# Kernel tuning notes

Hardware: AMD Instinct MI355X
Metric: run time of the kernel (lower is better)

## Reference

```python
import jax, jax.numpy as jnp
import numpy as np

B, C, H, W, K = 4, 64, 128, 128, 3
K2 = K * K
PAD = (K - 1) // 2  # same padding for 3x3


def setup_inputs() -> dict:
    key = jax.random.key(0)
    ks = jax.random.split(key, 9)
    s = 0.05
    return {
        "x": jax.random.normal(ks[0], (B, C, H, W), jnp.float32),
        "inter": jax.random.normal(ks[1], (B, C, H, W), jnp.float32),
        # offset/mask predictor conv: input cat([x, inter]) -> 3*K2 channels (dy, dx, mask)
        "w_offset": jax.random.normal(ks[2], (3 * K2, 2 * C, K, K), jnp.float32) * s,
        "b_offset": jnp.zeros((3 * K2,), jnp.float32),
        # deformable conv weight (bias=False per DGM init)
        "w_dcn": jax.random.normal(ks[3], (C, C, K, K), jnp.float32) * s,
        # SFT gamma branch: two 1x1 convs (bias=False)
        "w_g1": jax.random.normal(ks[4], (C, C), jnp.float32) * s,
        "w_g2": jax.random.normal(ks[5], (C, C), jnp.float32) * s,
        # SFT beta branch: two 1x1 convs (bias=False)
        "w_b1": jax.random.normal(ks[6], (C, C), jnp.float32) * s,
        "w_b2": jax.random.normal(ks[7], (C, C), jnp.float32) * s,
    }


def _lrelu(v):
    # LeakyReLU(0.1)
    return jnp.where(v >= 0, v, 0.1 * v)


def _conv(x, w, b=None):
    y = jax.lax.conv_general_dilated(
        x, w, window_strides=(1, 1), padding=[(PAD, PAD), (PAD, PAD)],
        dimension_numbers=("NCHW", "OIHW", "NCHW"))
    if b is not None:
        y = y + b[None, :, None, None]
    return y


def _bilinear_gather(x, py, px):
    """x: [B,C,H,W]; py, px: [B,K2,H,W] float sample coords.
    Returns samples [B,K2,H,W,C]; out-of-bounds treated as zero (DCN zero-pad)."""
    y0 = jnp.floor(py)
    x0 = jnp.floor(px)
    wy = (py - y0)[..., None]
    wx = (px - x0)[..., None]

    def gather(yi, xi):
        valid = ((yi >= 0) & (yi < H) & (xi >= 0) & (xi < W)).astype(x.dtype)
        yc = jnp.clip(yi, 0, H - 1).astype(jnp.int32)
        xc = jnp.clip(xi, 0, W - 1).astype(jnp.int32)
        bidx = jnp.arange(B)[:, None, None, None]
        v = x[bidx, :, yc, xc]  # advanced indexing -> [B,K2,H,W,C]
        return v * valid[..., None]

    v00 = gather(y0, x0)
    v01 = gather(y0, x0 + 1)
    v10 = gather(y0 + 1, x0)
    v11 = gather(y0 + 1, x0 + 1)
    return (v00 * (1 - wy) * (1 - wx) + v01 * (1 - wy) * wx
            + v10 * wy * (1 - wx) + v11 * wy * wx)


def _dgm_forward(x, inter, w_offset, b_offset, w_dcn, w_g1, w_g2, w_b1, w_b2):
    # --- WADCN branch: modulated deformable conv, offsets predicted from cat(x, inter)
    om = _conv(jnp.concatenate([x, inter], axis=1), w_offset, b_offset)  # [B,3K2,H,W]
    dy, dx, m = jnp.split(om, 3, axis=1)  # each [B,K2,H,W]
    mask = jax.nn.sigmoid(m)

    ky, kx = jnp.meshgrid(jnp.arange(K), jnp.arange(K), indexing="ij")
    ky = ky.reshape(K2).astype(x.dtype)
    kx = kx.reshape(K2).astype(x.dtype)
    hh = jnp.arange(H, dtype=x.dtype)
    ww = jnp.arange(W, dtype=x.dtype)
    # sample coords: base grid + kernel-tap offset + learned offset
    py = hh[None, None, :, None] + (ky - PAD)[None, :, None, None] + dy  # [B,K2,H,W]
    px = ww[None, None, None, :] + (kx - PAD)[None, :, None, None] + dx

    samp = _bilinear_gather(x, py, px) * mask[..., None]  # [B,K2,H,W,C]
    dcn_out = jnp.einsum("bkhwc,ock->bohw", samp, w_dcn.reshape(C, C, K2))

    # --- SFT branch: two 1x1-conv + LeakyReLU chains producing gamma/beta
    gamma = jnp.einsum("oc,bchw->bohw", w_g2,
                       _lrelu(jnp.einsum("oc,bchw->bohw", w_g1, inter)))
    beta = jnp.einsum("oc,bchw->bohw", w_b2,
                      _lrelu(jnp.einsum("oc,bchw->bohw", w_b1, inter)))
    sft_out = x * gamma + beta

    # --- fused residual combine (DGM.relu is defined but never applied)
    return x + dcn_out + sft_out


def reference(x, inter, w_offset, b_offset, w_dcn, w_g1, w_g2, w_b1, w_b2):
    return _dgm_forward(x, inter, w_offset, b_offset, w_dcn, w_g1, w_g2, w_b1, w_b2)
```

## Files before the change

kernel.cpp:

```cpp
#include <hip/hip_runtime.h>
#include <hip/hip_bf16.h>
#include <math.h>

#define BB 4
#define CC 64
#define HH 128
#define WW 128
#define HW (HH*WW)
#define NPIX (BB*HW)

typedef __attribute__((ext_vector_type(8))) short short8;
typedef __attribute__((ext_vector_type(4))) float f32x4;

__device__ __forceinline__ float bf2f(ushort u) {
  union { unsigned u; float f; } v; v.u = ((unsigned)u) << 16; return v.f;
}
__device__ __forceinline__ ushort f2bf(float f) {
  __hip_bfloat16 h = __float2bfloat16(f); return *(ushort*)&h;
}

__global__ __launch_bounds__(256) void k_prep(
    const float* __restrict__ x, const float* __restrict__ inter,
    const float* __restrict__ w_off, const float* __restrict__ w_dcn,
    const float* __restrict__ wg1, const float* __restrict__ wb1,
    const float* __restrict__ wg2, const float* __restrict__ wb2,
    ushort* __restrict__ x_clh, ushort* __restrict__ inter_clh,
    ushort* __restrict__ wfb, ushort* __restrict__ wdT,
    ushort* __restrict__ w1gb, ushort* __restrict__ w1bb,
    ushort* __restrict__ w2gb, ushort* __restrict__ w2bb,
    float* __restrict__ zp) {
  __shared__ __align__(16) float tile[64 * 128];
  int blk = blockIdx.x;
  int tid = threadIdx.x;
  if (blk < 1024) {
    int sel = blk >> 9;
    int bh = blk & 511;
    int b = bh >> 7, h = bh & 127;
    const float* src = sel ? inter : x;
    ushort* dst = sel ? inter_clh : x_clh;
    const float* sp = src + (size_t)(b * 64) * HW + h * WW;
#pragma unroll
    for (int it = 0; it < 8; ++it) {
      int idx = it * 256 + tid;
      int c = idx >> 5, wq = idx & 31;
      float4 v = *(const float4*)(sp + (size_t)c * HW + wq * 4);
      int s = (c >> 3) & 7;
      *(float4*)(&tile[c * 128 + ((wq ^ s) << 2)]) = v;
    }
    __syncthreads();
    ushort* dp = dst + ((size_t)b * HW + h * WW) * 64;
#pragma unroll
    for (int it = 0; it < 4; ++it) {
      int idx = it * 256 + tid;
      int w = idx >> 3, c8 = idx & 7;
      short8 outv;
#pragma unroll
      for (int j = 0; j < 8; ++j) {
        int c = c8 * 8 + j;
        int sl = (w >> 2) ^ c8;
        float f = tile[c * 128 + (sl << 2) + (w & 3)];
        outv[j] = (short)f2bf(f);
      }
      *(short8*)(dp + (size_t)w * 64 + c8 * 8) = outv;
    }
  } else if (blk < 1168) {
    int i = (blk - 1024) * 256 + tid;
    if (i < 64) zp[i] = 0.f;
    if (i < 9 * 32 * 128) {
      int tap = i >> 12, rem = i & 4095, m = rem >> 7, c = rem & 127;
      float v = (m < 27) ? w_off[(size_t)(m * 128 + c) * 9 + tap] : 0.f;
      wfb[i] = f2bf(v);
    }
  } else if (blk < 1312) {
    int i = (blk - 1168) * 256 + tid;
    if (i < 64 * 64 * 9) {
      int o = i / 576, rem = i % 576, k = rem >> 6, c = rem & 63;
      wdT[i] = f2bf(w_dcn[(o * 64 + c) * 9 + k]);
    }
  } else {
    int i = (blk - 1312) * 256 + tid;
    int m = i >> 12, j = i & 4095;
    const float* src = (m == 0) ? wg1 : (m == 1) ? wb1 : (m == 2) ? wg2 : wb2;
    ushort* dst = (m == 0) ? w1gb : (m == 1) ? w1bb : (m == 2) ? w2gb : w2bb;
    dst[j] = f2bf(src[j]);
  }
}

#define SPITCH 196
#define NPX 32
#define FPX 72

__global__ __launch_bounds__(256, 6) void k_omega(
    const float* __restrict__ x, const ushort* __restrict__ x_clh,
    const ushort* __restrict__ inter_clh,
    const float* __restrict__ b_off, const ushort* __restrict__ wfb,
    const ushort* __restrict__ wdT,
    const ushort* __restrict__ w1gb, const ushort* __restrict__ w1bb,
    const ushort* __restrict__ w2gb, const ushort* __restrict__ w2bb,
    const ushort* __restrict__ zp16, float* __restrict__ out) {
  __shared__ __align__(16) ushort LDSB[9792];
  ushort* S  = LDSB;
  ushort* Sg = LDSB;
  ushort* Sb = LDSB + NPX * FPX;
  int*   cycx = (int*)(LDSB + 6272);
  float* cwy  = (float*)(LDSB + 6848);
  float* cwx  = (float*)(LDSB + 7424);
  float* oml  = (float*)(LDSB + 8000);

  int tid = threadIdx.x;
  int wave = tid >> 6, lane = tid & 63;
  int quad = lane >> 4, col = lane & 15;
  int rr = lane >> 3, g = lane & 7;
  int bid = blockIdx.x;
  int wid = (bid & 7) * 256 + (bid >> 3);
  int pg0 = wid * NPX;
  int b = pg0 >> 14, hw0 = pg0 & 16383;
  int h = hw0 >> 7, w0 = hw0 & 127;
  int pt = wave >> 1, mt = wave & 1;
  int o_base = __builtin_amdgcn_readfirstlane(wave * 16);

  f32x4 accx = {0.f, 0.f, 0.f, 0.f}, acci = {0.f, 0.f, 0.f, 0.f};
  {
    const ushort* wb0 = wfb + (size_t)(mt * 16 + col) * 128 + quad * 8;
    int pxcol = pt * 16 + col;
    unsigned bbase = (unsigned)b * HW;
#pragma unroll 1
    for (int ky = 0; ky < 3; ++ky) {
      int hs = h + ky - 1;
      bool oky = (unsigned)hs < 128u;
      int rowb = hs << 7;
#pragma unroll
      for (int kx = 0; kx < 3; ++kx) {
        int ws = w0 + pxcol + kx - 1;
        bool ok = oky && ((unsigned)ws < 128u);
        long long poff = (long long)(int)(bbase + rowb + ws) * 64;
        const ushort* bx = (ok ? x_clh + poff : zp16) + quad * 8;
        const ushort* bi = (ok ? inter_clh + poff : zp16) + quad * 8;
        const ushort* wt = wb0 + (size_t)(ky * 3 + kx) * 4096;
#pragma unroll
        for (int ks = 0; ks < 2; ++ks) {
          short8 a0 = *(const short8*)(wt + ks * 32);
          short8 b0 = *(const short8*)(bx + ks * 32);
          accx = __builtin_amdgcn_mfma_f32_16x16x32_bf16(a0, b0, accx, 0, 0, 0);
          short8 a1 = *(const short8*)(wt + 64 + ks * 32);
          short8 b1 = *(const short8*)(bi + ks * 32);
          acci = __builtin_amdgcn_mfma_f32_16x16x32_bf16(a1, b1, acci, 0, 0, 0);
        }
      }
    }
  }
#pragma unroll
  for (int r = 0; r < 4; ++r) {
    int o = mt * 16 + quad * 4 + r;
    if (o < 27) oml[o * 33 + pt * 16 + col] = accx[r] + acci[r];
  }

  f32x4 ag[2], ab[2];
#pragma unroll
  for (int nt = 0; nt < 2; ++nt) {
    ag[nt] = (f32x4){0.f, 0.f, 0.f, 0.f};
    ab[nt] = (f32x4){0.f, 0.f, 0.f, 0.f};
  }
#pragma unroll
  for (int ks = 0; ks < 2; ++ks) {
    short8 a_g = *(const short8*)(w1gb + (size_t)(o_base + col) * 64 + ks * 32 + quad * 8);
    short8 a_b = *(const short8*)(w1bb + (size_t)(o_base + col) * 64 + ks * 32 + quad * 8);
#pragma unroll
    for (int nt = 0; nt < 2; ++nt) {
      short8 bf = *(const short8*)(inter_clh + (size_t)(pg0 + nt * 16 + col) * 64 + ks * 32 + quad * 8);
      ag[nt] = __builtin_amdgcn_mfma_f32_16x16x32_bf16(a_g, bf, ag[nt], 0, 0, 0);
      ab[nt] = __builtin_amdgcn_mfma_f32_16x16x32_bf16(a_b, bf, ab[nt], 0, 0, 0);
    }
  }
#pragma unroll
  for (int nt = 0; nt < 2; ++nt) {
    int px = nt * 16 + col;
    ushort pkg[4], pkb[4];
#pragma unroll
    for (int r = 0; r < 4; ++r) {
      float vg = ag[nt][r]; vg = vg >= 0.f ? vg : 0.1f * vg;
      float vb = ab[nt][r]; vb = vb >= 0.f ? vb : 0.1f * vb;
      pkg[r] = f2bf(vg); pkb[r] = f2bf(vb);
    }
    *(uint2*)(&Sg[px * FPX + o_base + quad * 4]) = *(uint2*)pkg;
    *(uint2*)(&Sb[px * FPX + o_base + quad * 4]) = *(uint2*)pkb;
  }
  __syncthreads();

  f32x4 gg[2], gb[2];
#pragma unroll
  for (int nt = 0; nt < 2; ++nt) {
    gg[nt] = (f32x4){0.f, 0.f, 0.f, 0.f};
    gb[nt] = (f32x4){0.f, 0.f, 0.f, 0.f};
  }
#pragma unroll
  for (int ks = 0; ks < 2; ++ks) {
    short8 a_g = *(const short8*)(w2gb + (size_t)(o_base + col) * 64 + ks * 32 + quad * 8);
    short8 a_b = *(const short8*)(w2bb + (size_t)(o_base + col) * 64 + ks * 32 + quad * 8);
#pragma unroll
    for (int nt = 0; nt < 2; ++nt) {
      short8 bgf = *(const short8*)(Sg + (nt * 16 + col) * FPX + ks * 32 + quad * 8);
      short8 bbf = *(const short8*)(Sb + (nt * 16 + col) * FPX + ks * 32 + quad * 8);
      gg[nt] = __builtin_amdgcn_mfma_f32_16x16x32_bf16(a_g, bgf, gg[nt], 0, 0, 0);
      gb[nt] = __builtin_amdgcn_mfma_f32_16x16x32_bf16(a_b, bbf, gb[nt], 0, 0, 0);
    }
  }
  float ev[2][4];
#pragma unroll
  for (int nt = 0; nt < 2; ++nt)
#pragma unroll
    for (int r = 0; r < 4; ++r) {
      int o = o_base + quad * 4 + r;
      float xv = x[(size_t)(b * 64 + o) * HW + hw0 + nt * 16 + col];
      ev[nt][r] = xv + xv * gg[nt][r] + gb[nt][r];
    }

  for (int i = tid; i < 9 * NPX; i += 256) {
    int k = i >> 5, p = i & 31;
    float dy = oml[k * 33 + p] + b_off[k];
    float dx = oml[(9 + k) * 33 + p] + b_off[9 + k];
    float mz = oml[(18 + k) * 33 + p] + b_off[18 + k];
    float py = (float)(h + (k / 3) - 1) + dy;
    float px = (float)(w0 + p + (k % 3) - 1) + dx;
    float y0f = floorf(py), x0f = floorf(px);
    int iy = (int)y0f, ix = (int)x0f;
    cycx[i] = (iy & 0xffff) | (ix << 16);
    cwy[i] = py - y0f;
    cwx[i] = px - x0f;
    oml[(18 + k) * 33 + p] = 1.f / (1.f + __expf(-mz));
  }

  f32x4 acc[2];
  acc[0] = (f32x4){0.f, 0.f, 0.f, 0.f};
  acc[1] = (f32x4){0.f, 0.f, 0.f, 0.f};

  const ushort* bp = x_clh + (size_t)b * HW * 64;
  int p = wave * 8 + rr;

#pragma unroll 1
  for (int chunk = 0; chunk < 3; ++chunk) {
    __syncthreads();
#pragma unroll
    for (int it = 0; it < 3; ++it) {
      int k = chunk * 3 + it;
      int idx = k * 32 + p;
      int v = cycx[idx];
      int y0 = (int)(short)(v & 0xffff);
      int x0 = v >> 16;
      float wy = cwy[idx], wx = cwx[idx];
      float m = oml[(18 + k) * 33 + p];
      bool yok0 = (unsigned)y0 < 128u, yok1 = (unsigned)(y0 + 1) < 128u;
      bool xok0 = (unsigned)x0 < 128u, xok1 = (unsigned)(x0 + 1) < 128u;
      const ushort* r0 = bp + ((size_t)(int)((y0 << 7) + x0)) * 64 + g * 8;
      const ushort* r1 = r0 + (size_t)WW * 64;
      short8 s00 = *(const short8*)((yok0 && xok0) ? r0 : zp16);
      short8 s01 = *(const short8*)((yok0 && xok1) ? (r0 + 64) : zp16);
      short8 s10 = *(const short8*)((yok1 && xok0) ? r1 : zp16);
      short8 s11 = *(const short8*)((yok1 && xok1) ? (r1 + 64) : zp16);
      short8 outv;
#pragma unroll
      for (int j = 0; j < 8; ++j) {
        float v00 = bf2f((ushort)s00[j]), v01 = bf2f((ushort)s01[j]);
        float v10 = bf2f((ushort)s10[j]), v11 = bf2f((ushort)s11[j]);
        float top = v00 + (v01 - v00) * wx;
        float bot = v10 + (v11 - v10) * wx;
        float val = top + (bot - top) * wy;
        outv[j] = (short)f2bf(val * m);
      }
      *(short8*)(&S[p * SPITCH + it * 64 + g * 8]) = outv;
    }
    __syncthreads();
    const ushort* wrow = wdT + (size_t)(o_base + col) * 576 + chunk * 192 + quad * 8;
    const ushort* srow = S + quad * 8;
#pragma unroll
    for (int ks = 0; ks < 6; ++ks) {
      short8 a = *(const short8*)(wrow + ks * 32);
#pragma unroll
      for (int nt = 0; nt < 2; ++nt) {
        short8 bf = *(const short8*)(srow + (nt * 16 + col) * SPITCH + ks * 32);
        acc[nt] = __builtin_amdgcn_mfma_f32_16x16x32_bf16(a, bf, acc[nt], 0, 0, 0);
      }
    }
  }

#pragma unroll
  for (int nt = 0; nt < 2; ++nt) {
#pragma unroll
    for (int r = 0; r < 4; ++r) {
      int o = o_base + quad * 4 + r;
      size_t idx = (size_t)(b * 64 + o) * HW + hw0 + nt * 16 + col;
      out[idx] = ev[nt][r] + acc[nt][r];
    }
  }
}

extern "C" void kernel_launch(void* const* d_in, const int* in_sizes, int n_in,
                              void* d_out, int out_size, void* d_ws, size_t ws_size,
                              hipStream_t stream) {
  const float* x     = (const float*)d_in[0];
  const float* inter = (const float*)d_in[1];
  const float* w_off = (const float*)d_in[2];
  const float* b_off = (const float*)d_in[3];
  const float* w_dcn = (const float*)d_in[4];
  const float* wg1   = (const float*)d_in[5];
  const float* wg2   = (const float*)d_in[6];
  const float* wb1   = (const float*)d_in[7];
  const float* wb2   = (const float*)d_in[8];
  float* out = (float*)d_out;

  float* ws        = (float*)d_ws;
  ushort* x_clh    = (ushort*)ws;
  ushort* inter_clh= (ushort*)(ws + 2097152);
  ushort* wfb      = (ushort*)(ws + 4194304);
  ushort* wdT      = (ushort*)(ws + 4212736);
  ushort* w1gb     = (ushort*)(ws + 4231168);
  ushort* w1bb     = (ushort*)(ws + 4233216);
  ushort* w2gb     = (ushort*)(ws + 4235264);
  ushort* w2bb     = (ushort*)(ws + 4237312);
  float* zp        = ws + 4239360;

  k_prep<<<1376, 256, 0, stream>>>(x, inter, w_off, w_dcn, wg1, wb1, wg2, wb2,
                                   x_clh, inter_clh, wfb, wdT,
                                   w1gb, w1bb, w2gb, w2bb, zp);

  k_omega<<<2048, 256, 0, stream>>>(x, x_clh, inter_clh, b_off, wfb, wdT,
                                    w1gb, w1bb, w2gb, w2bb,
                                    (const ushort*)zp, out);
}
```

Measured before the change: 204.1 us.

## Give each wave its own pixel tile and feed bilinear samples straight into MFMA

Each block now covers 64 pixels instead of 32, and each wave owns 16 pixels across all 64 output channels, where before the waves split the work by output channel. The bilinear samples are built in registers in the MFMA B-operand layout and consumed directly, which removes the LDS staging buffer and the per-chunk barriers in the deformable-conv loop. The offset conv and SFT stages are reorganised the same way, with fewer blocks and launch bounds reduced to 4 blocks per SIMD. The cost is more accumulator registers per wave and possibly lower occupancy, and every wave now reloads all the weight rows from global memory or cache.

```diff
diff --git a/kernel.cpp b/kernel.cpp
--- a/kernel.cpp
+++ b/kernel.cpp
@@ -86,11 +86,11 @@
   }
 }
 
-#define SPITCH 196
-#define NPX 32
-#define FPX 72
-
-__global__ __launch_bounds__(256, 6) void k_omega(
+#define NPX 64
+#define SGP 72
+#define OMP 66
+
+__global__ __launch_bounds__(256, 4) void k_omega(
     const float* __restrict__ x, const ushort* __restrict__ x_clh,
     const ushort* __restrict__ inter_clh,
     const float* __restrict__ b_off, const ushort* __restrict__ wfb,
@@ -98,200 +98,191 @@
     const ushort* __restrict__ w1gb, const ushort* __restrict__ w1bb,
     const ushort* __restrict__ w2gb, const ushort* __restrict__ w2bb,
     const ushort* __restrict__ zp16, float* __restrict__ out) {
-  __shared__ __align__(16) ushort LDSB[9792];
-  ushort* S  = LDSB;
+  __shared__ __align__(16) ushort LDSB[12780];
   ushort* Sg = LDSB;
-  ushort* Sb = LDSB + NPX * FPX;
-  int*   cycx = (int*)(LDSB + 6272);
-  float* cwy  = (float*)(LDSB + 6848);
-  float* cwx  = (float*)(LDSB + 7424);
-  float* oml  = (float*)(LDSB + 8000);
+  ushort* Sb = LDSB + 4608;
+  int*   cycx = (int*)LDSB;
+  float* cwy  = (float*)(LDSB + 1152);
+  float* cwx  = (float*)(LDSB + 2304);
+  float* oml  = (float*)(LDSB + 9216);
 
   int tid = threadIdx.x;
   int wave = tid >> 6, lane = tid & 63;
   int quad = lane >> 4, col = lane & 15;
-  int rr = lane >> 3, g = lane & 7;
   int bid = blockIdx.x;
-  int wid = (bid & 7) * 256 + (bid >> 3);
+  int wid = (bid & 7) * 128 + (bid >> 3);
   int pg0 = wid * NPX;
   int b = pg0 >> 14, hw0 = pg0 & 16383;
   int h = hw0 >> 7, w0 = hw0 & 127;
-  int pt = wave >> 1, mt = wave & 1;
-  int o_base = __builtin_amdgcn_readfirstlane(wave * 16);
-
-  f32x4 accx = {0.f, 0.f, 0.f, 0.f}, acci = {0.f, 0.f, 0.f, 0.f};
+  int pxl = wave * 16 + col;
+  int pxg = pg0 + pxl;
+
+  f32x4 am0 = {0.f, 0.f, 0.f, 0.f}, am1 = {0.f, 0.f, 0.f, 0.f};
   {
-    const ushort* wb0 = wfb + (size_t)(mt * 16 + col) * 128 + quad * 8;
-    int pxcol = pt * 16 + col;
+    const ushort* wb0 = wfb + (size_t)col * 128 + quad * 8;
+    const ushort* wb1 = wfb + (size_t)(16 + col) * 128 + quad * 8;
     unsigned bbase = (unsigned)b * HW;
-#pragma unroll 1
+#pragma unroll
     for (int ky = 0; ky < 3; ++ky) {
       int hs = h + ky - 1;
       bool oky = (unsigned)hs < 128u;
       int rowb = hs << 7;
 #pragma unroll
       for (int kx = 0; kx < 3; ++kx) {
-        int ws = w0 + pxcol + kx - 1;
+        int ws = w0 + pxl + kx - 1;
         bool ok = oky && ((unsigned)ws < 128u);
         long long poff = (long long)(int)(bbase + rowb + ws) * 64;
         const ushort* bx = (ok ? x_clh + poff : zp16) + quad * 8;
         const ushort* bi = (ok ? inter_clh + poff : zp16) + quad * 8;
-        const ushort* wt = wb0 + (size_t)(ky * 3 + kx) * 4096;
+        int tap = ky * 3 + kx;
+        const ushort* wt0 = wb0 + (size_t)tap * 4096;
+        const ushort* wt1 = wb1 + (size_t)tap * 4096;
 #pragma unroll
         for (int ks = 0; ks < 2; ++ks) {
-          short8 a0 = *(const short8*)(wt + ks * 32);
           short8 b0 = *(const short8*)(bx + ks * 32);
-          accx = __builtin_amdgcn_mfma_f32_16x16x32_bf16(a0, b0, accx, 0, 0, 0);
-          short8 a1 = *(const short8*)(wt + 64 + ks * 32);
           short8 b1 = *(const short8*)(bi + ks * 32);
-          acci = __builtin_amdgcn_mfma_f32_16x16x32_bf16(a1, b1, acci, 0, 0, 0);
+          am0 = __builtin_amdgcn_mfma_f32_16x16x32_bf16(*(const short8*)(wt0 + ks * 32), b0, am0, 0, 0, 0);
+          am0 = __builtin_amdgcn_mfma_f32_16x16x32_bf16(*(const short8*)(wt0 + 64 + ks * 32), b1, am0, 0, 0, 0);
+          am1 = __builtin_amdgcn_mfma_f32_16x16x32_bf16(*(const short8*)(wt1 + ks * 32), b0, am1, 0, 0, 0);
+          am1 = __builtin_amdgcn_mfma_f32_16x16x32_bf16(*(const short8*)(wt1 + 64 + ks * 32), b1, am1, 0, 0, 0);
         }
       }
     }
   }
 #pragma unroll
   for (int r = 0; r < 4; ++r) {
-    int o = mt * 16 + quad * 4 + r;
-    if (o < 27) oml[o * 33 + pt * 16 + col] = accx[r] + acci[r];
-  }
-
-  f32x4 ag[2], ab[2];
-#pragma unroll
-  for (int nt = 0; nt < 2; ++nt) {
-    ag[nt] = (f32x4){0.f, 0.f, 0.f, 0.f};
-    ab[nt] = (f32x4){0.f, 0.f, 0.f, 0.f};
+    int m0 = quad * 4 + r;
+    oml[m0 * OMP + pxl] = am0[r];
+    int m1 = 16 + quad * 4 + r;
+    if (m1 < 27) oml[m1 * OMP + pxl] = am1[r];
+  }
+
+  f32x4 ag[4], ab[4];
+#pragma unroll
+  for (int og = 0; og < 4; ++og) {
+    ag[og] = (f32x4){0.f, 0.f, 0.f, 0.f};
+    ab[og] = (f32x4){0.f, 0.f, 0.f, 0.f};
   }
 #pragma unroll
   for (int ks = 0; ks < 2; ++ks) {
-    short8 a_g = *(const short8*)(w1gb + (size_t)(o_base + col) * 64 + ks * 32 + quad * 8);
-    short8 a_b = *(const short8*)(w1bb + (size_t)(o_base + col) * 64 + ks * 32 + quad * 8);
-#pragma unroll
-    for (int nt = 0; nt < 2; ++nt) {
-      short8 bf = *(const short8*)(inter_clh + (size_t)(pg0 + nt * 16 + col) * 64 + ks * 32 + quad * 8);
-      ag[nt] = __builtin_amdgcn_mfma_f32_16x16x32_bf16(a_g, bf, ag[nt], 0, 0, 0);
-      ab[nt] = __builtin_amdgcn_mfma_f32_16x16x32_bf16(a_b, bf, ab[nt], 0, 0, 0);
-    }
-  }
-#pragma unroll
-  for (int nt = 0; nt < 2; ++nt) {
-    int px = nt * 16 + col;
+    short8 bf = *(const short8*)(inter_clh + (size_t)pxg * 64 + ks * 32 + quad * 8);
+#pragma unroll
+    for (int og = 0; og < 4; ++og) {
+      short8 a_g = *(const short8*)(w1gb + (size_t)(og * 16 + col) * 64 + ks * 32 + quad * 8);
+      short8 a_b = *(const short8*)(w1bb + (size_t)(og * 16 + col) * 64 + ks * 32 + quad * 8);
+      ag[og] = __builtin_amdgcn_mfma_f32_16x16x32_bf16(a_g, bf, ag[og], 0, 0, 0);
+      ab[og] = __builtin_amdgcn_mfma_f32_16x16x32_bf16(a_b, bf, ab[og], 0, 0, 0);
+    }
+  }
+#pragma unroll
+  for (int og = 0; og < 4; ++og) {
     ushort pkg[4], pkb[4];
 #pragma unroll
     for (int r = 0; r < 4; ++r) {
-      float vg = ag[nt][r]; vg = vg >= 0.f ? vg : 0.1f * vg;
-      float vb = ab[nt][r]; vb = vb >= 0.f ? vb : 0.1f * vb;
+      float vg = ag[og][r]; vg = vg >= 0.f ? vg : 0.1f * vg;
+      float vb = ab[og][r]; vb = vb >= 0.f ? vb : 0.1f * vb;
       pkg[r] = f2bf(vg); pkb[r] = f2bf(vb);
     }
-    *(uint2*)(&Sg[px * FPX + o_base + quad * 4]) = *(uint2*)pkg;
-    *(uint2*)(&Sb[px * FPX + o_base + quad * 4]) = *(uint2*)pkb;
+    *(uint2*)(&Sg[pxl * SGP + og * 16 + quad * 4]) = *(uint2*)pkg;
+    *(uint2*)(&Sb[pxl * SGP + og * 16 + quad * 4]) = *(uint2*)pkb;
   }
   __syncthreads();
 
-  f32x4 gg[2], gb[2];
-#pragma unroll
-  for (int nt = 0; nt < 2; ++nt) {
-    gg[nt] = (f32x4){0.f, 0.f, 0.f, 0.f};
-    gb[nt] = (f32x4){0.f, 0.f, 0.f, 0.f};
+  f32x4 gg[4], gb[4];
+#pragma unroll
+  for (int og = 0; og < 4; ++og) {
+    gg[og] = (f32x4){0.f, 0.f, 0.f, 0.f};
+    gb[og] = (f32x4){0.f, 0.f, 0.f, 0.f};
   }
 #pragma unroll
   for (int ks = 0; ks < 2; ++ks) {
-    short8 a_g = *(const short8*)(w2gb + (size_t)(o_base + col) * 64 + ks * 32 + quad * 8);
-    short8 a_b = *(const short8*)(w2bb + (size_t)(o_base + col) * 64 + ks * 32 + quad * 8);
-#pragma unroll
-    for (int nt = 0; nt < 2; ++nt) {
-      short8 bgf = *(const short8*)(Sg + (nt * 16 + col) * FPX + ks * 32 + quad * 8);
-      short8 bbf = *(const short8*)(Sb + (nt * 16 + col) * FPX + ks * 32 + quad * 8);
-      gg[nt] = __builtin_amdgcn_mfma_f32_16x16x32_bf16(a_g, bgf, gg[nt], 0, 0, 0);
-      gb[nt] = __builtin_amdgcn_mfma_f32_16x16x32_bf16(a_b, bbf, gb[nt], 0, 0, 0);
-    }
-  }
-  float ev[2][4];
-#pragma unroll
-  for (int nt = 0; nt < 2; ++nt)
+    short8 bgf = *(const short8*)(Sg + pxl * SGP + ks * 32 + quad * 8);
+    short8 bbf = *(const short8*)(Sb + pxl * SGP + ks * 32 + quad * 8);
+#pragma unroll
+    for (int og = 0; og < 4; ++og) {
+      short8 a_g = *(const short8*)(w2gb + (size_t)(og * 16 + col) * 64 + ks * 32 + quad * 8);
+      short8 a_b = *(const short8*)(w2bb + (size_t)(og * 16 + col) * 64 + ks * 32 + quad * 8);
+      gg[og] = __builtin_amdgcn_mfma_f32_16x16x32_bf16(a_g, bgf, gg[og], 0, 0, 0);
+      gb[og] = __builtin_amdgcn_mfma_f32_16x16x32_bf16(a_b, bbf, gb[og], 0, 0, 0);
+    }
+  }
+  float ev[4][4];
+#pragma unroll
+  for (int og = 0; og < 4; ++og)
 #pragma unroll
     for (int r = 0; r < 4; ++r) {
-      int o = o_base + quad * 4 + r;
-      float xv = x[(size_t)(b * 64 + o) * HW + hw0 + nt * 16 + col];
-      ev[nt][r] = xv + xv * gg[nt][r] + gb[nt][r];
-    }
+      int o = og * 16 + quad * 4 + r;
+      float xv = x[(size_t)(b * 64 + o) * HW + hw0 + pxl];
+      ev[og][r] = xv + xv * gg[og][r] + gb[og][r];
+    }
+  __syncthreads();
 
   for (int i = tid; i < 9 * NPX; i += 256) {
-    int k = i >> 5, p = i & 31;
-    float dy = oml[k * 33 + p] + b_off[k];
-    float dx = oml[(9 + k) * 33 + p] + b_off[9 + k];
-    float mz = oml[(18 + k) * 33 + p] + b_off[18 + k];
-    float py = (float)(h + (k / 3) - 1) + dy;
-    float px = (float)(w0 + p + (k % 3) - 1) + dx;
+    int t = i >> 6, p = i & 63;
+    float dy = oml[t * OMP + p] + b_off[t];
+    float dx = oml[(9 + t) * OMP + p] + b_off[9 + t];
+    float mz = oml[(18 + t) * OMP + p] + b_off[18 + t];
+    float py = (float)(h + (t / 3) - 1) + dy;
+    float px = (float)(w0 + p + (t % 3) - 1) + dx;
     float y0f = floorf(py), x0f = floorf(px);
     int iy = (int)y0f, ix = (int)x0f;
     cycx[i] = (iy & 0xffff) | (ix << 16);
     cwy[i] = py - y0f;
     cwx[i] = px - x0f;
-    oml[(18 + k) * 33 + p] = 1.f / (1.f + __expf(-mz));
-  }
-
-  f32x4 acc[2];
-  acc[0] = (f32x4){0.f, 0.f, 0.f, 0.f};
-  acc[1] = (f32x4){0.f, 0.f, 0.f, 0.f};
-
-  const ushort* bp = x_clh + (size_t)b * HW * 64;
-  int p = wave * 8 + rr;
-
+    oml[(18 + t) * OMP + p] = 1.f / (1.f + __expf(-mz));
+  }
+  __syncthreads();
+
+  f32x4 acc[4];
+#pragma unroll
+  for (int og = 0; og < 4; ++og) acc[og] = (f32x4){0.f, 0.f, 0.f, 0.f};
+
+  const ushort* bp = x_clh + (size_t)b * HW * 64 + quad * 8;
 #pragma unroll 1
-  for (int chunk = 0; chunk < 3; ++chunk) {
-    __syncthreads();
-#pragma unroll
-    for (int it = 0; it < 3; ++it) {
-      int k = chunk * 3 + it;
-      int idx = k * 32 + p;
-      int v = cycx[idx];
-      int y0 = (int)(short)(v & 0xffff);
-      int x0 = v >> 16;
-      float wy = cwy[idx], wx = cwx[idx];
-      float m = oml[(18 + k) * 33 + p];
-      bool yok0 = (unsigned)y0 < 128u, yok1 = (unsigned)(y0 + 1) < 128u;
-      bool xok0 = (unsigned)x0 < 128u, xok1 = (unsigned)(x0 + 1) < 128u;
-      const ushort* r0 = bp + ((size_t)(int)((y0 << 7) + x0)) * 64 + g * 8;
-      const ushort* r1 = r0 + (size_t)WW * 64;
-      short8 s00 = *(const short8*)((yok0 && xok0) ? r0 : zp16);
-      short8 s01 = *(const short8*)((yok0 && xok1) ? (r0 + 64) : zp16);
-      short8 s10 = *(const short8*)((yok1 && xok0) ? r1 : zp16);
-      short8 s11 = *(const short8*)((yok1 && xok1) ? (r1 + 64) : zp16);
-      short8 outv;
+  for (int t = 0; t < 9; ++t) {
+    int idx = t * 64 + pxl;
+    int v = cycx[idx];
+    int y0 = (int)(short)(v & 0xffff);
+    int x0 = v >> 16;
+    float wy = cwy[idx], wxx = cwx[idx];
+    float m = oml[(18 + t) * OMP + pxl];
+    bool yok0 = (unsigned)y0 < 128u, yok1 = (unsigned)(y0 + 1) < 128u;
+    bool xok0 = (unsigned)x0 < 128u, xok1 = (unsigned)(x0 + 1) < 128u;
+    const ushort* r0 = bp + (long long)(int)((y0 << 7) + x0) * 64;
+    const ushort* r1 = r0 + (size_t)WW * 64;
+#pragma unroll
+    for (int h2 = 0; h2 < 2; ++h2) {
+      int off = h2 * 32;
+      short8 s00 = *(const short8*)((yok0 && xok0) ? (r0 + off) : (zp16 + off));
+      short8 s01 = *(const short8*)((yok0 && xok1) ? (r0 + 64 + off) : (zp16 + off));
+      short8 s10 = *(const short8*)((yok1 && xok0) ? (r1 + off) : (zp16 + off));
+      short8 s11 = *(const short8*)((yok1 && xok1) ? (r1 + 64 + off) : (zp16 + off));
+      short8 bfr;
 #pragma unroll
       for (int j = 0; j < 8; ++j) {
         float v00 = bf2f((ushort)s00[j]), v01 = bf2f((ushort)s01[j]);
         float v10 = bf2f((ushort)s10[j]), v11 = bf2f((ushort)s11[j]);
-        float top = v00 + (v01 - v00) * wx;
-        float bot = v10 + (v11 - v10) * wx;
+        float top = v00 + (v01 - v00) * wxx;
+        float bot = v10 + (v11 - v10) * wxx;
         float val = top + (bot - top) * wy;
-        outv[j] = (short)f2bf(val * m);
+        bfr[j] = (short)f2bf(val * m);
       }
-      *(short8*)(&S[p * SPITCH + it * 64 + g * 8]) = outv;
-    }
-    __syncthreads();
-    const ushort* wrow = wdT + (size_t)(o_base + col) * 576 + chunk * 192 + quad * 8;
-    const ushort* srow = S + quad * 8;
-#pragma unroll
-    for (int ks = 0; ks < 6; ++ks) {
-      short8 a = *(const short8*)(wrow + ks * 32);
-#pragma unroll
-      for (int nt = 0; nt < 2; ++nt) {
-        short8 bf = *(const short8*)(srow + (nt * 16 + col) * SPITCH + ks * 32);
-        acc[nt] = __builtin_amdgcn_mfma_f32_16x16x32_bf16(a, bf, acc[nt], 0, 0, 0);
+#pragma unroll
+      for (int og = 0; og < 4; ++og) {
+        short8 a = *(const short8*)(wdT + (size_t)(og * 16 + col) * 576 + t * 64 + off + quad * 8);
+        acc[og] = __builtin_amdgcn_mfma_f32_16x16x32_bf16(a, bfr, acc[og], 0, 0, 0);
       }
     }
   }
 
 #pragma unroll
-  for (int nt = 0; nt < 2; ++nt) {
+  for (int og = 0; og < 4; ++og)
 #pragma unroll
     for (int r = 0; r < 4; ++r) {
-      int o = o_base + quad * 4 + r;
-      size_t idx = (size_t)(b * 64 + o) * HW + hw0 + nt * 16 + col;
-      out[idx] = ev[nt][r] + acc[nt][r];
-    }
-  }
+      int o = og * 16 + quad * 4 + r;
+      size_t idx = (size_t)(b * 64 + o) * HW + hw0 + pxl;
+      out[idx] = ev[og][r] + acc[og][r];
+    }
 }
 
 extern "C" void kernel_launch(void* const* d_in, const int* in_sizes, int n_in,
@@ -323,7 +314,7 @@
                                    x_clh, inter_clh, wfb, wdT,
                                    w1gb, w1bb, w2gb, w2bb, zp);
 
-  k_omega<<<2048, 256, 0, stream>>>(x, x_clh, inter_clh, b_off, wfb, wdT,
+  k_omega<<<1024, 256, 0, stream>>>(x, x_clh, inter_clh, b_off, wfb, wdT,
                                     w1gb, w1bb, w2gb, w2bb,
                                     (const ushort*)zp, out);
 }
```

Result: slower. 227.9 us (+11.7%).
